# Kernel tuning notes

Hardware: AMD Instinct MI355X
Metric: run time of the kernel (lower is better)

## Reference

```python
import jax, jax.numpy as jnp
import numpy as np

N_HEADS = 16


def _rope(x, cos, sin):
    # x: (B,H,S,hd); cos,sin: (1,1,S,hd//2). Full-dim rotation (rot_dim == head_dim).
    xe = x[..., 0::2]
    xo = x[..., 1::2]
    re = xe * cos - xo * sin
    ro = xe * sin + xo * cos
    return jnp.stack([re, ro], axis=-1).reshape(x.shape)


def setup_inputs() -> dict:
    key = jax.random.key(0)
    B, S, D = 2, 2048, 1024
    hd = D // N_HEADS
    k1, k2, k3, k4, k5 = jax.random.split(key, 5)
    x = jax.random.normal(k1, (B, S, D), dtype=jnp.float32)
    # Linear params (lecun-normal-ish scale)
    w_qkv = jax.random.normal(k2, (D, 3 * D), dtype=jnp.float32) / np.sqrt(D)
    b_qkv = jnp.zeros((3 * D,), dtype=jnp.float32)
    w_out = jax.random.normal(k3, (D, D), dtype=jnp.float32) / np.sqrt(D)
    b_out = jnp.zeros((D,), dtype=jnp.float32)
    # Rotary tables: (S, hd//2)
    inv_freq = 1.0 / (10000.0 ** (np.arange(0, hd, 2, dtype=np.float32) / hd))
    angles = jnp.asarray(np.arange(S, dtype=np.float32)[:, None] * inv_freq[None, :])
    cos = jnp.cos(angles)
    sin = jnp.sin(angles)
    # Causal mask (seq, seq), True = attend
    mask = jnp.tril(jnp.ones((S, S), dtype=bool))
    return {"x": x, "w_qkv": w_qkv, "b_qkv": b_qkv, "w_out": w_out,
            "b_out": b_out, "cos": cos, "sin": sin, "mask": mask}


def reference(x, w_qkv, b_qkv, w_out, b_out, cos, sin, mask):
    B, S, D = x.shape
    H = N_HEADS
    hd = D // H
    scale = hd ** (-0.5)
    qkv = x @ w_qkv + b_qkv  # (B,S,3D)
    qkv = qkv.reshape(B, S, 3, H, hd).transpose(2, 0, 3, 1, 4)  # (3,B,H,S,hd)
    q, k, v = qkv[0], qkv[1], qkv[2]
    c = cos[None, None, :, :]
    s = sin[None, None, :, :]
    q = _rope(q, c, s)
    k = _rope(k, c, s)
    attn = jnp.einsum('bhqd,bhkd->bhqk', q, k) * scale
    attn = jnp.where(mask, attn, -1e9)
    attn = jax.nn.softmax(attn, axis=-1)
    out = jnp.einsum('bhqk,bhkd->bhqd', attn, v)
    out = out.transpose(0, 2, 1, 3).reshape(B, S, D)
    return out @ w_out + b_out
```

## Files before the change

kernel.cpp:

```cpp
#include <hip/hip_runtime.h>
#include <stdint.h>

typedef unsigned short u16;
typedef __attribute__((ext_vector_type(8))) __bf16 bf16x8;
typedef __attribute__((ext_vector_type(4))) float f32x4;
typedef __attribute__((ext_vector_type(4))) unsigned short u16x4;

__device__ __forceinline__ float bf2f(u16 u){
  unsigned int x = ((unsigned int)u) << 16;
  return __builtin_bit_cast(float, x);
}
__device__ __forceinline__ u16 f2bf(float f){
  return __builtin_bit_cast(u16, (__bf16)f);
}
__device__ __forceinline__ float fexp2(float x){ return __builtin_exp2f(x); }
__device__ __forceinline__ void lds_load16(const void* g, void* l){
  __builtin_amdgcn_global_load_lds(
      (const __attribute__((address_space(1))) unsigned int*)g,
      (__attribute__((address_space(3))) unsigned int*)l, 16, 0, 0);
}

__device__ __forceinline__ void transpose_body(const float* __restrict__ in,
                                               u16* __restrict__ out,
                                               int R, int C, int bx, int by,
                                               u16 (*t)[65]){
  const int c0 = bx * 64, r0 = by * 64;
  const int tid = threadIdx.x;
  const int rr = tid >> 3;
  const int cc = (tid & 7) * 8;
#pragma unroll
  for (int i = 0; i < 2; i++){
    int r = i * 32 + rr;
    const float* p = in + (size_t)(r0 + r) * C + c0 + cc;
    f32x4 v0 = *(const f32x4*)p;
    f32x4 v1 = *(const f32x4*)(p + 4);
#pragma unroll
    for (int j = 0; j < 4; j++){ t[r][cc + j] = f2bf(v0[j]); t[r][cc + 4 + j] = f2bf(v1[j]); }
  }
  __syncthreads();
#pragma unroll
  for (int i = 0; i < 2; i++){
    int c = i * 32 + rr;
    u16 tmp[8];
#pragma unroll
    for (int j = 0; j < 8; j++) tmp[j] = t[cc + j][c];
    *(bf16x8*)(out + (size_t)(c0 + c) * R + r0 + cc) = *(const bf16x8*)tmp;
  }
}

__global__ __launch_bounds__(256) void prep(const float* __restrict__ w_qkv,
                                            const float* __restrict__ w_out,
                                            const float* __restrict__ x,
                                            u16* __restrict__ wT1,
                                            u16* __restrict__ wT2,
                                            u16* __restrict__ xbf){
  __shared__ u16 t[64][65];
  const int bid = blockIdx.x;
  if (bid < 2048){
    int i = bid * 256 + threadIdx.x;
    const float* p = x + (size_t)i * 8;
    f32x4 v0 = *(const f32x4*)p;
    f32x4 v1 = *(const f32x4*)(p + 4);
    u16 tmp[8];
#pragma unroll
    for (int j = 0; j < 4; j++){ tmp[j] = f2bf(v0[j]); tmp[4 + j] = f2bf(v1[j]); }
    *(bf16x8*)(xbf + (size_t)i * 8) = *(const bf16x8*)tmp;
  } else if (bid < 2048 + 768){
    int idx = bid - 2048;
    transpose_body(w_qkv, wT1, 1024, 3072, idx % 48, idx / 48, t);
  } else {
    int idx = bid - 2816;
    transpose_body(w_out, wT2, 1024, 1024, idx % 16, idx / 16, t);
  }
}

__global__ __launch_bounds__(256) void v_transpose(const u16* __restrict__ qkv,
                                                   u16* __restrict__ vT){
  const int S = 2048, LD = 3072;
  __shared__ u16 t[64][65];
  const int bh = blockIdx.y;
  const int b = bh >> 4, h = bh & 15;
  const int s0 = blockIdx.x * 64;
  const u16* src = qkv + (size_t)b * S * LD + 2048 + h * 64;
  const int tid = threadIdx.x;
  const int rr = tid >> 3;
  const int cc = (tid & 7) * 8;
#pragma unroll
  for (int i = 0; i < 2; i++){
    int s = i * 32 + rr;
    bf16x8 v = *(const bf16x8*)(src + (size_t)(s0 + s) * LD + cc);
#pragma unroll
    for (int j = 0; j < 8; j++) t[s][cc + j] = __builtin_bit_cast(u16, (__bf16)v[j]);
  }
  __syncthreads();
  u16* dst = vT + (size_t)bh * 64 * S;
#pragma unroll
  for (int i = 0; i < 2; i++){
    int d = i * 32 + rr;
    u16 tmp[8];
#pragma unroll
    for (int j = 0; j < 8; j++) tmp[j] = t[cc + j][d];
    *(bf16x8*)(dst + (size_t)d * S + s0 + cc) = *(const bf16x8*)tmp;
  }
}

template<bool OUTF32, bool ROPE>
__global__ __launch_bounds__(256, 3) void gemm_bt(const u16* __restrict__ A,
                                                  const u16* __restrict__ Bt,
                                                  const float* __restrict__ bias,
                                                  void* __restrict__ Cv,
                                                  int M, int N, int K,
                                                  const float* __restrict__ cosb,
                                                  const float* __restrict__ sinb){
  __shared__ u16 As[128 * 32];
  __shared__ u16 Bs[128 * 32];
  const int nx = gridDim.x;
  const int L = blockIdx.x + nx * blockIdx.y;
  const int per = (nx * gridDim.y) >> 3;
  const int wg = (L & 7) * per + (L >> 3);
  const int bn = wg % nx, bm = wg / nx;
  const int tid = threadIdx.x, w = tid >> 6, l = tid & 63;
  const int lo = l & 15, hi = l >> 4;
  const int wr = (w >> 1) * 64, wc = (w & 1) * 64;
  f32x4 acc[4][4] = {};
  const int lrow = l >> 2, lcd = l & 3;

  for (int k0 = 0; k0 < K; k0 += 32){
#pragma unroll
    for (int i = 0; i < 2; i++){
      int row0 = i * 64 + w * 16;
      int row = row0 + lrow;
      int cs = lcd ^ ((row >> 1) & 3);
      lds_load16(A  + (size_t)(bm * 128 + row) * K + k0 + cs * 8,
                 (char*)As + row0 * 64);
      lds_load16(Bt + (size_t)(bn * 128 + row) * K + k0 + cs * 8,
                 (char*)Bs + row0 * 64);
    }
    __syncthreads();
    bf16x8 a[4], b[4];
#pragma unroll
    for (int mi = 0; mi < 4; mi++){
      int row = wr + mi * 16 + lo;
      unsigned byte = (unsigned)(row * 64 + hi * 16) ^ (((row >> 1) & 3) << 4);
      a[mi] = *(const bf16x8*)((const char*)As + byte);
    }
#pragma unroll
    for (int ni = 0; ni < 4; ni++){
      int row = wc + ni * 16 + lo;
      unsigned byte = (unsigned)(row * 64 + hi * 16) ^ (((row >> 1) & 3) << 4);
      b[ni] = *(const bf16x8*)((const char*)Bs + byte);
    }
    __builtin_amdgcn_s_setprio(1);
#pragma unroll
    for (int mi = 0; mi < 4; mi++)
#pragma unroll
      for (int ni = 0; ni < 4; ni++)
        acc[mi][ni] = __builtin_amdgcn_mfma_f32_16x16x32_bf16(a[mi], b[ni], acc[mi][ni], 0, 0, 0);
    __builtin_amdgcn_s_setprio(0);
    __syncthreads();
  }
  if (ROPE && bn < 16){
#pragma unroll
    for (int mi = 0; mi < 4; mi++){
#pragma unroll
      for (int r = 0; r < 4; r++){
        int grow = bm * 128 + wr + mi * 16 + hi * 4 + r;
        int stok = grow & 2047;
#pragma unroll
        for (int ni = 0; ni < 4; ni++){
          int col = bn * 128 + wc + ni * 16 + lo;
          float v = acc[mi][ni][r] + bias[col];
          float partner = __shfl_xor(v, 1, 64);
          int ip = (col & 63) >> 1;
          float c = cosb[stok * 32 + ip], sn = sinb[stok * 32 + ip];
          float res = (lo & 1) ? (partner * sn + v * c) : (v * c - partner * sn);
          ((u16*)Cv)[(size_t)grow * N + col] = f2bf(res);
        }
      }
    }
  } else {
#pragma unroll
    for (int mi = 0; mi < 4; mi++){
#pragma unroll
      for (int r = 0; r < 4; r++){
        int grow = bm * 128 + wr + mi * 16 + hi * 4 + r;
#pragma unroll
        for (int ni = 0; ni < 4; ni++){
          int col = bn * 128 + wc + ni * 16 + lo;
          float v = acc[mi][ni][r] + bias[col];
          if (OUTF32)
            ((float*)Cv)[(size_t)grow * N + col] = v;
          else
            ((u16*)Cv)[(size_t)grow * N + col] = f2bf(v);
        }
      }
    }
  }
}

#define FA_DSREAD(KB_, KT_)                                                    \
  { _Pragma("unroll")                                                          \
    for (int c = 0; c < 2; c++){                                               \
      _Pragma("unroll")                                                        \
      for (int f = 0; f < 2; f++){                                             \
        int srw = f * 16 + lo;                                                 \
        unsigned byte = ((unsigned)(srw * 128 + c * 64 + hi * 16)) ^           \
                        ((lo & 7) << 4);                                       \
        KB_[c * 2 + f] = *(const bf16x8*)(                                     \
            (const char*)&Ks[w][(KT_) & 1][0] + byte);                         \
      } } }

#define FA_STAGE(KT_)                                                          \
  { _Pragma("unroll")                                                          \
    for (int i = 0; i < 4; i++)                                                \
      lds_load16(Kp + (size_t)((KT_) * 32 + i * 8 + srow8) * LD + scs * 8,     \
                 (char*)&Ks[w][(KT_) & 1][0] + i * 1024); }

#define FA_BODY(KBU_, KBL_, KT_, OA_, OB_, MA_, MB_)                           \
  {                                                                            \
    bf16x8 vb[4];                                                              \
    _Pragma("unroll")                                                          \
    for (int fd = 0; fd < 4; fd++)                                             \
      vb[fd] = *(const bf16x8*)(Vb + (size_t)(fd * 16 + lo) * S +              \
                                (KT_) * 32 + hi * 8);                          \
    if ((KT_) + 1 < k1) FA_DSREAD(KBL_, (KT_) + 1);                            \
    f32x4 saA[2] = {}, saB[2] = {};                                            \
    __builtin_amdgcn_s_setprio(1);                                             \
    saA[0] = __builtin_amdgcn_mfma_f32_16x16x32_bf16(KBU_[0], qfA0, saA[0], 0, 0, 0); \
    saB[0] = __builtin_amdgcn_mfma_f32_16x16x32_bf16(KBU_[0], qfB0, saB[0], 0, 0, 0); \
    saA[0] = __builtin_amdgcn_mfma_f32_16x16x32_bf16(KBU_[2], qfA1, saA[0], 0, 0, 0); \
    saB[0] = __builtin_amdgcn_mfma_f32_16x16x32_bf16(KBU_[2], qfB1, saB[0], 0, 0, 0); \
    saA[1] = __builtin_amdgcn_mfma_f32_16x16x32_bf16(KBU_[1], qfA0, saA[1], 0, 0, 0); \
    saB[1] = __builtin_amdgcn_mfma_f32_16x16x32_bf16(KBU_[1], qfB0, saB[1], 0, 0, 0); \
    saA[1] = __builtin_amdgcn_mfma_f32_16x16x32_bf16(KBU_[3], qfA1, saA[1], 0, 0, 0); \
    saB[1] = __builtin_amdgcn_mfma_f32_16x16x32_bf16(KBU_[3], qfB1, saB[1], 0, 0, 0); \
    __builtin_amdgcn_s_setprio(0);                                             \
    __builtin_amdgcn_sched_barrier(0);                                         \
    if ((KT_) + 2 < k1) FA_STAGE((KT_) + 2);                                   \
    if ((KT_) == nkt - 1){                                                     \
      _Pragma("unroll")                                                        \
      for (int f = 0; f < 2; f++){                                             \
        int key0 = (KT_) * 32 + f * 16 + hi * 4;                               \
        _Pragma("unroll")                                                      \
        for (int r = 0; r < 4; r++){                                           \
          if (key0 + r > qrA) saA[f][r] = -1e30f;                              \
          if (key0 + r > qrB) saB[f][r] = -1e30f;                              \
        }                                                                      \
      }                                                                        \
    }                                                                          \
    float pmA = fmaxf(                                                         \
        fmaxf(fmaxf(saA[0][0], saA[0][1]), fmaxf(saA[0][2], saA[0][3])),       \
        fmaxf(fmaxf(saA[1][0], saA[1][1]), fmaxf(saA[1][2], saA[1][3])));      \
    float pmB = fmaxf(                                                         \
        fmaxf(fmaxf(saB[0][0], saB[0][1]), fmaxf(saB[0][2], saB[0][3])),       \
        fmaxf(fmaxf(saB[1][0], saB[1][1]), fmaxf(saB[1][2], saB[1][3])));      \
    if (!__all(fmaxf(pmA - MA_, pmB - MB_) <= 11.5f)){                         \
      float rmA = fmaxf(pmA, __shfl_xor(pmA, 16, 64));                         \
      rmA = fmaxf(rmA, __shfl_xor(rmA, 32, 64));                               \
      float rmB = fmaxf(pmB, __shfl_xor(pmB, 16, 64));                         \
      rmB = fmaxf(rmB, __shfl_xor(rmB, 32, 64));                               \
      float mnA = fmaxf(MA_, rmA), mnB = fmaxf(MB_, rmB);                      \
      float cA = fexp2(MA_ - mnA), cB = fexp2(MB_ - mnB);                      \
      MA_ = mnA; MB_ = mnB;                                                    \
      lparA *= cA; lparB *= cB;                                                \
      float cqA[4], cqB[4];                                                    \
      _Pragma("unroll")                                                        \
      for (int r = 0; r < 4; r++){                                             \
        cqA[r] = __shfl(cA, hi * 4 + r, 64);                                   \
        cqB[r] = __shfl(cB, hi * 4 + r, 64);                                   \
      }                                                                        \
      _Pragma("unroll")                                                        \
      for (int fd = 0; fd < 4; fd++){                                          \
        _Pragma("unroll")                                                      \
        for (int r = 0; r < 4; r++){                                           \
          OA_[fd][r] *= cqA[r]; OB_[fd][r] *= cqB[r];                          \
        }                                                                      \
      }                                                                        \
    }                                                                          \
    float pvA[2][4], pvB[2][4];                                                \
    _Pragma("unroll")                                                          \
    for (int f = 0; f < 2; f++){                                               \
      _Pragma("unroll")                                                        \
      for (int r = 0; r < 4; r++){                                             \
        pvA[f][r] = fexp2(saA[f][r] - MA_);                                    \
        pvB[f][r] = fexp2(saB[f][r] - MB_);                                    \
      }                                                                        \
    }                                                                          \
    _Pragma("unroll")                                                          \
    for (int f = 0; f < 2; f++){                                               \
      u16x4 pkA, pkB;                                                          \
      _Pragma("unroll")                                                        \
      for (int r = 0; r < 4; r++){                                             \
        pkA[r] = f2bf(pvA[f][r]); pkB[r] = f2bf(pvB[f][r]);                    \
      }                                                                        \
      *(u16x4*)((char*)&Ps[w][0][0] + lo * 72 + f * 32 + hi * 8) = pkA;        \
      *(u16x4*)((char*)&Ps[w][1][0] + lo * 72 + f * 32 + hi * 8) = pkB;        \
    }                                                                          \
    lparA += ((pvA[0][0] + pvA[0][1]) + (pvA[0][2] + pvA[0][3]))               \
           + ((pvA[1][0] + pvA[1][1]) + (pvA[1][2] + pvA[1][3]));              \
    lparB += ((pvB[0][0] + pvB[0][1]) + (pvB[0][2] + pvB[0][3]))               \
           + ((pvB[1][0] + pvB[1][1]) + (pvB[1][2] + pvB[1][3]));              \
    bf16x8 paA = *(const bf16x8*)((const char*)&Ps[w][0][0] + lo * 72 +        \
                                  hi * 16);                                    \
    bf16x8 paB = *(const bf16x8*)((const char*)&Ps[w][1][0] + lo * 72 +        \
                                  hi * 16);                                    \
    __builtin_amdgcn_s_setprio(1);                                             \
    _Pragma("unroll")                                                          \
    for (int fd = 0; fd < 4; fd++){                                            \
      OA_[fd] = __builtin_amdgcn_mfma_f32_16x16x32_bf16(paA, vb[fd],           \
                                                        OA_[fd], 0, 0, 0);     \
      OB_[fd] = __builtin_amdgcn_mfma_f32_16x16x32_bf16(paB, vb[fd],           \
                                                        OB_[fd], 0, 0, 0);     \
    }                                                                          \
    __builtin_amdgcn_s_setprio(0);                                             \
  }

#define FA_PHASE(T_, OA_, OB_, MA_, MB_, LA_, LB_)                             \
  {                                                                            \
    const int q0p = (T_) * 32;                                                 \
    const int qrA = q0p + lo, qrB = q0p + 16 + lo;                             \
    const int nkt = (T_) + 1;                                                  \
    const int ch = (nkt + 1) >> 1;                                             \
    const int k0 = w ? ch : 0;                                                 \
    const int k1 = w ? nkt : ch;                                               \
    bf16x8 qfA0, qfA1, qfB0, qfB1;                                             \
    {                                                                          \
      bf16x8 va0 = *(const bf16x8*)(Qp + (size_t)qrA * LD + hi * 8);           \
      bf16x8 va1 = *(const bf16x8*)(Qp + (size_t)qrA * LD + 32 + hi * 8);      \
      bf16x8 vb0 = *(const bf16x8*)(Qp + (size_t)qrB * LD + hi * 8);           \
      bf16x8 vb1 = *(const bf16x8*)(Qp + (size_t)qrB * LD + 32 + hi * 8);      \
      _Pragma("unroll")                                                        \
      for (int j = 0; j < 8; j++){                                             \
        qfA0[j] = (__bf16)((float)va0[j] * QSC);                               \
        qfA1[j] = (__bf16)((float)va1[j] * QSC);                               \
        qfB0[j] = (__bf16)((float)vb0[j] * QSC);                               \
        qfB1[j] = (__bf16)((float)vb1[j] * QSC);                               \
      }                                                                        \
    }                                                                          \
    float lparA = 0.f, lparB = 0.f;                                            \
    MA_ = -1e30f; MB_ = -1e30f;                                                \
    bf16x8 kbA[4], kbB[4];                                                     \
    int kt = k0;                                                               \
    if (kt < k1){                                                              \
      FA_STAGE(kt);                                                            \
      if (kt + 1 < k1) FA_STAGE(kt + 1);                                       \
      FA_DSREAD(kbA, kt);                                                      \
      while (true){                                                            \
        FA_BODY(kbA, kbB, kt, OA_, OB_, MA_, MB_);                             \
        kt++;                                                                  \
        if (kt >= k1) break;                                                   \
        FA_BODY(kbB, kbA, kt, OA_, OB_, MA_, MB_);                             \
        kt++;                                                                  \
        if (kt >= k1) break;                                                   \
      }                                                                        \
    }                                                                          \
    lparA += __shfl_xor(lparA, 16, 64); lparA += __shfl_xor(lparA, 32, 64);    \
    lparB += __shfl_xor(lparB, 16, 64); lparB += __shfl_xor(lparB, 32, 64);    \
    LA_ = lparA; LB_ = lparB;                                                  \
  }

#define FA_WRITEPART(slot_, OA_, OB_, MA_, MB_, LA_, LB_)                      \
  {                                                                            \
    _Pragma("unroll")                                                          \
    for (int fd = 0; fd < 4; fd++){                                            \
      u16x4 pkA, pkB;                                                          \
      _Pragma("unroll")                                                        \
      for (int r = 0; r < 4; r++){                                             \
        pkA[r] = f2bf(OA_[fd][r]); pkB[r] = f2bf(OB_[fd][r]);                  \
      }                                                                        \
      *(u16x4*)((char*)&Xo[slot_][0] + (fd * 16 + lo) * 72 + hi * 8) = pkA;    \
      *(u16x4*)((char*)&Xo[slot_][0] + (fd * 16 + lo) * 72 + 32 + hi * 8) = pkB;\
    }                                                                          \
    if (hi == 0){                                                              \
      Xm[slot_][lo] = MA_;      Xl[slot_][lo] = LA_;                           \
      Xm[slot_][16 + lo] = MB_; Xl[slot_][16 + lo] = LB_;                      \
    }                                                                          \
  }

#define FA_COMBINE(slot_, T_, OA_, OB_, MA_, MB_, LA_, LB_)                    \
  {                                                                            \
    const int q0p = (T_) * 32;                                                 \
    u16x4 pA[4], pB[4];                                                        \
    _Pragma("unroll")                                                          \
    for (int fd = 0; fd < 4; fd++){                                            \
      pA[fd] = *(const u16x4*)((const char*)&Xo[slot_][0] +                    \
                               (fd * 16 + lo) * 72 + hi * 8);                  \
      pB[fd] = *(const u16x4*)((const char*)&Xo[slot_][0] +                    \
                               (fd * 16 + lo) * 72 + 32 + hi * 8);             \
    }                                                                          \
    _Pragma("unroll")                                                          \
    for (int r = 0; r < 4; r++){                                               \
      float mOA = __shfl(MA_, hi * 4 + r, 64);                                 \
      float lOA = __shfl(LA_, hi * 4 + r, 64);                                 \
      float mOB = __shfl(MB_, hi * 4 + r, 64);                                 \
      float lOB = __shfl(LB_, hi * 4 + r, 64);                                 \
      float mPA = Xm[slot_][hi * 4 + r], lPA = Xl[slot_][hi * 4 + r];          \
      float mPB = Xm[slot_][16 + hi * 4 + r], lPB = Xl[slot_][16 + hi * 4 + r];\
      float MfA = fmaxf(mOA, mPA), MfB = fmaxf(mOB, mPB);                      \
      float c0A = fexp2(mOA - MfA), c1A = fexp2(mPA - MfA);                    \
      float c0B = fexp2(mOB - MfB), c1B = fexp2(mPB - MfB);                    \
      float invA = 1.0f / (lOA * c0A + lPA * c1A);                             \
      float invB = 1.0f / (lOB * c0B + lPB * c1B);                             \
      int srA = q0p + hi * 4 + r;                                              \
      int srB = q0p + 16 + hi * 4 + r;                                         \
      u16* orA = Oout + (size_t)(b * S + srA) * 1024 + h * 64;                 \
      u16* orB = Oout + (size_t)(b * S + srB) * 1024 + h * 64;                 \
      _Pragma("unroll")                                                        \
      for (int fd = 0; fd < 4; fd++){                                          \
        float vA = (OA_[fd][r] * c0A + bf2f(pA[fd][r]) * c1A) * invA;          \
        float vB = (OB_[fd][r] * c0B + bf2f(pB[fd][r]) * c1B) * invB;          \
        orA[fd * 16 + lo] = f2bf(vA);                                          \
        orB[fd * 16 + lo] = f2bf(vB);                                          \
      }                                                                        \
    }                                                                          \
  }

__global__ __launch_bounds__(128, 2) void flash_attn(const u16* __restrict__ qkv,
                                                     const u16* __restrict__ vT,
                                                     u16* __restrict__ Oout){
  const int S = 2048, LD = 3072;
  const int L = blockIdx.x;
  const int bh = L & 31;
  const int bx = L >> 5;
  const int b = bh >> 4, h = bh & 15;
  const u16* base = qkv + (size_t)b * S * LD;
  const u16* Qp = base + h * 64;
  const u16* Kp = base + 1024 + h * 64;
  const u16* Vb = vT + (size_t)bh * 64 * S;
  const int tid = threadIdx.x, w = tid >> 6, l = tid & 63;
  const int lo = l & 15, hi = l >> 4;
  __shared__ u16 Ks[2][2][32 * 64];
  __shared__ u16 Ps[2][2][16 * 36];
  __shared__ u16 Xo[2][64 * 36];
  __shared__ float Xm[2][32], Xl[2][32];

  const float QSC = 0.125f * 1.44269504089f;
  const int srow8 = l >> 3;
  const int scs = (l & 7) ^ srow8;

  f32x4 o1A[4] = {}, o1B[4] = {};
  f32x4 o2A[4] = {}, o2B[4] = {};
  float m1A, m1B, l1A, l1B, m2A, m2B, l2A, l2B;

  FA_PHASE(63 - bx, o1A, o1B, m1A, m1B, l1A, l1B);
  if (w == 1) FA_WRITEPART(0, o1A, o1B, m1A, m1B, l1A, l1B);
  FA_PHASE(bx,      o2A, o2B, m2A, m2B, l2A, l2B);
  if (w == 0) FA_WRITEPART(1, o2A, o2B, m2A, m2B, l2A, l2B);
  __syncthreads();
  if (w == 0){
    FA_COMBINE(0, 63 - bx, o1A, o1B, m1A, m1B, l1A, l1B);
  } else {
    FA_COMBINE(1, bx,      o2A, o2B, m2A, m2B, l2A, l2B);
  }
}

extern "C" void kernel_launch(void* const* d_in, const int* in_sizes, int n_in,
                              void* d_out, int out_size, void* d_ws, size_t ws_size,
                              hipStream_t stream){
  const float* x     = (const float*)d_in[0];
  const float* w_qkv = (const float*)d_in[1];
  const float* b_qkv = (const float*)d_in[2];
  const float* w_out = (const float*)d_in[3];
  const float* b_out = (const float*)d_in[4];
  const float* cosb  = (const float*)d_in[5];
  const float* sinb  = (const float*)d_in[6];
  float* out = (float*)d_out;
  char* ws = (char*)d_ws;
  u16* qkv  = (u16*)(ws);
  u16* attn = (u16*)(ws + 25165824);
  u16* xbf  = attn;
  u16* wT2  = (u16*)(ws + 33554432);
  u16* wT1  = (u16*)(ws + 35651584);
  u16* vT   = (u16*)(ws + 35651584);

  prep<<<3072, 256, 0, stream>>>(w_qkv, w_out, x, wT1, wT2, xbf);
  gemm_bt<false, true ><<<dim3(24, 32), 256, 0, stream>>>(xbf, wT1, b_qkv, qkv,
                                                          4096, 3072, 1024, cosb, sinb);
  v_transpose<<<dim3(32, 32), 256, 0, stream>>>(qkv, vT);
  flash_attn<<<1024, 128, 0, stream>>>(qkv, vT, attn);
  gemm_bt<true , false><<<dim3(8, 32), 256, 0, stream>>>(attn, wT2, b_out, out,
                                                         4096, 1024, 1024, cosb, sinb);
}
```

Before: 124.3 us.

## Split paired causal query tiles into separate blocks with higher occupancy

```diff
diff --git a/kernel.cpp b/kernel.cpp
--- a/kernel.cpp
+++ b/kernel.cpp
@@ -216,7 +216,7 @@
       lds_load16(Kp + (size_t)((KT_) * 32 + i * 8 + srow8) * LD + scs * 8,     \
                  (char*)&Ks[w][(KT_) & 1][0] + i * 1024); }
 
-#define FA_BODY(KBU_, KBL_, KT_, OA_, OB_, MA_, MB_)                           \
+#define FA_BODY(KBU_, KBL_, KT_)                                               \
   {                                                                            \
     bf16x8 vb[4];                                                              \
     _Pragma("unroll")                                                          \
@@ -254,14 +254,14 @@
     float pmB = fmaxf(                                                         \
         fmaxf(fmaxf(saB[0][0], saB[0][1]), fmaxf(saB[0][2], saB[0][3])),       \
         fmaxf(fmaxf(saB[1][0], saB[1][1]), fmaxf(saB[1][2], saB[1][3])));      \
-    if (!__all(fmaxf(pmA - MA_, pmB - MB_) <= 11.5f)){                         \
+    if (!__all(fmaxf(pmA - mA, pmB - mB) <= 11.5f)){                           \
       float rmA = fmaxf(pmA, __shfl_xor(pmA, 16, 64));                         \
       rmA = fmaxf(rmA, __shfl_xor(rmA, 32, 64));                               \
       float rmB = fmaxf(pmB, __shfl_xor(pmB, 16, 64));                         \
       rmB = fmaxf(rmB, __shfl_xor(rmB, 32, 64));                               \
-      float mnA = fmaxf(MA_, rmA), mnB = fmaxf(MB_, rmB);                      \
-      float cA = fexp2(MA_ - mnA), cB = fexp2(MB_ - mnB);                      \
-      MA_ = mnA; MB_ = mnB;                                                    \
+      float mnA = fmaxf(mA, rmA), mnB = fmaxf(mB, rmB);                        \
+      float cA = fexp2(mA - mnA), cB = fexp2(mB - mnB);                        \
+      mA = mnA; mB = mnB;                                                      \
       lparA *= cA; lparB *= cB;                                                \
       float cqA[4], cqB[4];                                                    \
       _Pragma("unroll")                                                        \
@@ -273,7 +273,7 @@
       for (int fd = 0; fd < 4; fd++){                                          \
         _Pragma("unroll")                                                      \
         for (int r = 0; r < 4; r++){                                           \
-          OA_[fd][r] *= cqA[r]; OB_[fd][r] *= cqB[r];                          \
+          oA[fd][r] *= cqA[r]; oB[fd][r] *= cqB[r];                            \
         }                                                                      \
       }                                                                        \
     }                                                                          \
@@ -282,8 +282,8 @@
     for (int f = 0; f < 2; f++){                                               \
       _Pragma("unroll")                                                        \
       for (int r = 0; r < 4; r++){                                             \
-        pvA[f][r] = fexp2(saA[f][r] - MA_);                                    \
-        pvB[f][r] = fexp2(saB[f][r] - MB_);                                    \
+        pvA[f][r] = fexp2(saA[f][r] - mA);                                     \
+        pvB[f][r] = fexp2(saB[f][r] - mB);                                     \
       }                                                                        \
     }                                                                          \
     _Pragma("unroll")                                                          \
@@ -307,121 +307,21 @@
     __builtin_amdgcn_s_setprio(1);                                             \
     _Pragma("unroll")                                                          \
     for (int fd = 0; fd < 4; fd++){                                            \
-      OA_[fd] = __builtin_amdgcn_mfma_f32_16x16x32_bf16(paA, vb[fd],           \
-                                                        OA_[fd], 0, 0, 0);     \
-      OB_[fd] = __builtin_amdgcn_mfma_f32_16x16x32_bf16(paB, vb[fd],           \
-                                                        OB_[fd], 0, 0, 0);     \
+      oA[fd] = __builtin_amdgcn_mfma_f32_16x16x32_bf16(paA, vb[fd],            \
+                                                       oA[fd], 0, 0, 0);       \
+      oB[fd] = __builtin_amdgcn_mfma_f32_16x16x32_bf16(paB, vb[fd],            \
+                                                       oB[fd], 0, 0, 0);       \
     }                                                                          \
     __builtin_amdgcn_s_setprio(0);                                             \
   }
 
-#define FA_PHASE(T_, OA_, OB_, MA_, MB_, LA_, LB_)                             \
-  {                                                                            \
-    const int q0p = (T_) * 32;                                                 \
-    const int qrA = q0p + lo, qrB = q0p + 16 + lo;                             \
-    const int nkt = (T_) + 1;                                                  \
-    const int ch = (nkt + 1) >> 1;                                             \
-    const int k0 = w ? ch : 0;                                                 \
-    const int k1 = w ? nkt : ch;                                               \
-    bf16x8 qfA0, qfA1, qfB0, qfB1;                                             \
-    {                                                                          \
-      bf16x8 va0 = *(const bf16x8*)(Qp + (size_t)qrA * LD + hi * 8);           \
-      bf16x8 va1 = *(const bf16x8*)(Qp + (size_t)qrA * LD + 32 + hi * 8);      \
-      bf16x8 vb0 = *(const bf16x8*)(Qp + (size_t)qrB * LD + hi * 8);           \
-      bf16x8 vb1 = *(const bf16x8*)(Qp + (size_t)qrB * LD + 32 + hi * 8);      \
-      _Pragma("unroll")                                                        \
-      for (int j = 0; j < 8; j++){                                             \
-        qfA0[j] = (__bf16)((float)va0[j] * QSC);                               \
-        qfA1[j] = (__bf16)((float)va1[j] * QSC);                               \
-        qfB0[j] = (__bf16)((float)vb0[j] * QSC);                               \
-        qfB1[j] = (__bf16)((float)vb1[j] * QSC);                               \
-      }                                                                        \
-    }                                                                          \
-    float lparA = 0.f, lparB = 0.f;                                            \
-    MA_ = -1e30f; MB_ = -1e30f;                                                \
-    bf16x8 kbA[4], kbB[4];                                                     \
-    int kt = k0;                                                               \
-    if (kt < k1){                                                              \
-      FA_STAGE(kt);                                                            \
-      if (kt + 1 < k1) FA_STAGE(kt + 1);                                       \
-      FA_DSREAD(kbA, kt);                                                      \
-      while (true){                                                            \
-        FA_BODY(kbA, kbB, kt, OA_, OB_, MA_, MB_);                             \
-        kt++;                                                                  \
-        if (kt >= k1) break;                                                   \
-        FA_BODY(kbB, kbA, kt, OA_, OB_, MA_, MB_);                             \
-        kt++;                                                                  \
-        if (kt >= k1) break;                                                   \
-      }                                                                        \
-    }                                                                          \
-    lparA += __shfl_xor(lparA, 16, 64); lparA += __shfl_xor(lparA, 32, 64);    \
-    lparB += __shfl_xor(lparB, 16, 64); lparB += __shfl_xor(lparB, 32, 64);    \
-    LA_ = lparA; LB_ = lparB;                                                  \
-  }
-
-#define FA_WRITEPART(slot_, OA_, OB_, MA_, MB_, LA_, LB_)                      \
-  {                                                                            \
-    _Pragma("unroll")                                                          \
-    for (int fd = 0; fd < 4; fd++){                                            \
-      u16x4 pkA, pkB;                                                          \
-      _Pragma("unroll")                                                        \
-      for (int r = 0; r < 4; r++){                                             \
-        pkA[r] = f2bf(OA_[fd][r]); pkB[r] = f2bf(OB_[fd][r]);                  \
-      }                                                                        \
-      *(u16x4*)((char*)&Xo[slot_][0] + (fd * 16 + lo) * 72 + hi * 8) = pkA;    \
-      *(u16x4*)((char*)&Xo[slot_][0] + (fd * 16 + lo) * 72 + 32 + hi * 8) = pkB;\
-    }                                                                          \
-    if (hi == 0){                                                              \
-      Xm[slot_][lo] = MA_;      Xl[slot_][lo] = LA_;                           \
-      Xm[slot_][16 + lo] = MB_; Xl[slot_][16 + lo] = LB_;                      \
-    }                                                                          \
-  }
-
-#define FA_COMBINE(slot_, T_, OA_, OB_, MA_, MB_, LA_, LB_)                    \
-  {                                                                            \
-    const int q0p = (T_) * 32;                                                 \
-    u16x4 pA[4], pB[4];                                                        \
-    _Pragma("unroll")                                                          \
-    for (int fd = 0; fd < 4; fd++){                                            \
-      pA[fd] = *(const u16x4*)((const char*)&Xo[slot_][0] +                    \
-                               (fd * 16 + lo) * 72 + hi * 8);                  \
-      pB[fd] = *(const u16x4*)((const char*)&Xo[slot_][0] +                    \
-                               (fd * 16 + lo) * 72 + 32 + hi * 8);             \
-    }                                                                          \
-    _Pragma("unroll")                                                          \
-    for (int r = 0; r < 4; r++){                                               \
-      float mOA = __shfl(MA_, hi * 4 + r, 64);                                 \
-      float lOA = __shfl(LA_, hi * 4 + r, 64);                                 \
-      float mOB = __shfl(MB_, hi * 4 + r, 64);                                 \
-      float lOB = __shfl(LB_, hi * 4 + r, 64);                                 \
-      float mPA = Xm[slot_][hi * 4 + r], lPA = Xl[slot_][hi * 4 + r];          \
-      float mPB = Xm[slot_][16 + hi * 4 + r], lPB = Xl[slot_][16 + hi * 4 + r];\
-      float MfA = fmaxf(mOA, mPA), MfB = fmaxf(mOB, mPB);                      \
-      float c0A = fexp2(mOA - MfA), c1A = fexp2(mPA - MfA);                    \
-      float c0B = fexp2(mOB - MfB), c1B = fexp2(mPB - MfB);                    \
-      float invA = 1.0f / (lOA * c0A + lPA * c1A);                             \
-      float invB = 1.0f / (lOB * c0B + lPB * c1B);                             \
-      int srA = q0p + hi * 4 + r;                                              \
-      int srB = q0p + 16 + hi * 4 + r;                                         \
-      u16* orA = Oout + (size_t)(b * S + srA) * 1024 + h * 64;                 \
-      u16* orB = Oout + (size_t)(b * S + srB) * 1024 + h * 64;                 \
-      _Pragma("unroll")                                                        \
-      for (int fd = 0; fd < 4; fd++){                                          \
-        float vA = (OA_[fd][r] * c0A + bf2f(pA[fd][r]) * c1A) * invA;          \
-        float vB = (OB_[fd][r] * c0B + bf2f(pB[fd][r]) * c1B) * invB;          \
-        orA[fd * 16 + lo] = f2bf(vA);                                          \
-        orB[fd * 16 + lo] = f2bf(vB);                                          \
-      }                                                                        \
-    }                                                                          \
-  }
-
-__global__ __launch_bounds__(128, 2) void flash_attn(const u16* __restrict__ qkv,
+__global__ __launch_bounds__(128, 3) void flash_attn(const u16* __restrict__ qkv,
                                                      const u16* __restrict__ vT,
                                                      u16* __restrict__ Oout){
   const int S = 2048, LD = 3072;
   const int L = blockIdx.x;
   const int bh = L & 31;
-  const int bx = L >> 5;
+  const int T = 63 - (L >> 5);
   const int b = bh >> 4, h = bh & 15;
   const u16* base = qkv + (size_t)b * S * LD;
   const u16* Qp = base + h * 64;
@@ -431,26 +331,105 @@
   const int lo = l & 15, hi = l >> 4;
   __shared__ u16 Ks[2][2][32 * 64];
   __shared__ u16 Ps[2][2][16 * 36];
-  __shared__ u16 Xo[2][64 * 36];
-  __shared__ float Xm[2][32], Xl[2][32];
+  __shared__ u16 Xo[64 * 36];
+  __shared__ float Xm[32], Xl[32];
 
   const float QSC = 0.125f * 1.44269504089f;
   const int srow8 = l >> 3;
   const int scs = (l & 7) ^ srow8;
 
-  f32x4 o1A[4] = {}, o1B[4] = {};
-  f32x4 o2A[4] = {}, o2B[4] = {};
-  float m1A, m1B, l1A, l1B, m2A, m2B, l2A, l2B;
-
-  FA_PHASE(63 - bx, o1A, o1B, m1A, m1B, l1A, l1B);
-  if (w == 1) FA_WRITEPART(0, o1A, o1B, m1A, m1B, l1A, l1B);
-  FA_PHASE(bx,      o2A, o2B, m2A, m2B, l2A, l2B);
-  if (w == 0) FA_WRITEPART(1, o2A, o2B, m2A, m2B, l2A, l2B);
+  const int q0 = T * 32;
+  const int qrA = q0 + lo, qrB = q0 + 16 + lo;
+  const int nkt = T + 1;
+  const int ch = (nkt + 1) >> 1;
+  const int k0 = w ? ch : 0;
+  const int k1 = w ? nkt : ch;
+
+  bf16x8 qfA0, qfA1, qfB0, qfB1;
+  {
+    bf16x8 va0 = *(const bf16x8*)(Qp + (size_t)qrA * LD + hi * 8);
+    bf16x8 va1 = *(const bf16x8*)(Qp + (size_t)qrA * LD + 32 + hi * 8);
+    bf16x8 vb0 = *(const bf16x8*)(Qp + (size_t)qrB * LD + hi * 8);
+    bf16x8 vb1 = *(const bf16x8*)(Qp + (size_t)qrB * LD + 32 + hi * 8);
+#pragma unroll
+    for (int j = 0; j < 8; j++){
+      qfA0[j] = (__bf16)((float)va0[j] * QSC);
+      qfA1[j] = (__bf16)((float)va1[j] * QSC);
+      qfB0[j] = (__bf16)((float)vb0[j] * QSC);
+      qfB1[j] = (__bf16)((float)vb1[j] * QSC);
+    }
+  }
+
+  f32x4 oA[4] = {}, oB[4] = {};
+  float mA = -1e30f, mB = -1e30f;
+  float lparA = 0.f, lparB = 0.f;
+
+  bf16x8 kbA[4], kbB[4];
+  int kt = k0;
+  if (kt < k1){
+    FA_STAGE(kt);
+    if (kt + 1 < k1) FA_STAGE(kt + 1);
+    FA_DSREAD(kbA, kt);
+    while (true){
+      FA_BODY(kbA, kbB, kt);
+      kt++;
+      if (kt >= k1) break;
+      FA_BODY(kbB, kbA, kt);
+      kt++;
+      if (kt >= k1) break;
+    }
+  }
+  lparA += __shfl_xor(lparA, 16, 64); lparA += __shfl_xor(lparA, 32, 64);
+  lparB += __shfl_xor(lparB, 16, 64); lparB += __shfl_xor(lparB, 32, 64);
+
+  __syncthreads();
+  if (w == 1){
+#pragma unroll
+    for (int fd = 0; fd < 4; fd++){
+      u16x4 pkA, pkB;
+#pragma unroll
+      for (int r = 0; r < 4; r++){ pkA[r] = f2bf(oA[fd][r]); pkB[r] = f2bf(oB[fd][r]); }
+      *(u16x4*)((char*)Xo + (fd * 16 + lo) * 72 + hi * 8) = pkA;
+      *(u16x4*)((char*)Xo + (fd * 16 + lo) * 72 + 32 + hi * 8) = pkB;
+    }
+    if (hi == 0){
+      Xm[lo] = mA;      Xl[lo] = lparA;
+      Xm[16 + lo] = mB; Xl[16 + lo] = lparB;
+    }
+  }
   __syncthreads();
   if (w == 0){
-    FA_COMBINE(0, 63 - bx, o1A, o1B, m1A, m1B, l1A, l1B);
-  } else {
-    FA_COMBINE(1, bx,      o2A, o2B, m2A, m2B, l2A, l2B);
+    u16x4 pA[4], pB[4];
+#pragma unroll
+    for (int fd = 0; fd < 4; fd++){
+      pA[fd] = *(const u16x4*)((const char*)Xo + (fd * 16 + lo) * 72 + hi * 8);
+      pB[fd] = *(const u16x4*)((const char*)Xo + (fd * 16 + lo) * 72 + 32 + hi * 8);
+    }
+#pragma unroll
+    for (int r = 0; r < 4; r++){
+      float mOA = __shfl(mA, hi * 4 + r, 64);
+      float lOA = __shfl(lparA, hi * 4 + r, 64);
+      float mOB = __shfl(mB, hi * 4 + r, 64);
+      float lOB = __shfl(lparB, hi * 4 + r, 64);
+      float mPA = Xm[hi * 4 + r], lPA = Xl[hi * 4 + r];
+      float mPB = Xm[16 + hi * 4 + r], lPB = Xl[16 + hi * 4 + r];
+      float MfA = fmaxf(mOA, mPA), MfB = fmaxf(mOB, mPB);
+      float c0A = fexp2(mOA - MfA), c1A = fexp2(mPA - MfA);
+      float c0B = fexp2(mOB - MfB), c1B = fexp2(mPB - MfB);
+      float invA = 1.0f / (lOA * c0A + lPA * c1A);
+      float invB = 1.0f / (lOB * c0B + lPB * c1B);
+      int srA = q0 + hi * 4 + r;
+      int srB = q0 + 16 + hi * 4 + r;
+      u16* orA = Oout + (size_t)(b * S + srA) * 1024 + h * 64;
+      u16* orB = Oout + (size_t)(b * S + srB) * 1024 + h * 64;
+#pragma unroll
+      for (int fd = 0; fd < 4; fd++){
+        float vA = (oA[fd][r] * c0A + bf2f(pA[fd][r]) * c1A) * invA;
+        float vB = (oB[fd][r] * c0B + bf2f(pB[fd][r]) * c1B) * invB;
+        orA[fd * 16 + lo] = f2bf(vA);
+        orB[fd * 16 + lo] = f2bf(vB);
+      }
+    }
   }
 }
 
@@ -477,7 +456,7 @@
   gemm_bt<false, true ><<<dim3(24, 32), 256, 0, stream>>>(xbf, wT1, b_qkv, qkv,
                                                           4096, 3072, 1024, cosb, sinb);
   v_transpose<<<dim3(32, 32), 256, 0, stream>>>(qkv, vT);
-  flash_attn<<<1024, 128, 0, stream>>>(qkv, vT, attn);
+  flash_attn<<<2048, 128, 0, stream>>>(qkv, vT, attn);
   gemm_bt<true , false><<<dim3(8, 32), 256, 0, stream>>>(attn, wT2, b_out, out,
                                                          4096, 1024, 1024, cosb, sinb);
 }
```

Result: slower. 171.1 us (+37.7%).
